# Performance work log

Measured on AMD Instinct MI355X. Metric: run time of the kernel, lower is better.

Reference implementation:

```python
import jax, jax.numpy as jnp
import numpy as np

H = 64
N_TYPES = 20
EDGE_DIM = 4
N_GRAPHS = 128
N_LAYERS = 3
N_NODES = 50000
N_EDGES = 800000
NQ = 4

# ---- quantum-circuit constants (4 qubits, statevector of 16) ----
def _cnot_mat(c, t, n=NQ):
    m = np.zeros((2**n, 2**n), np.complex64)
    for i in range(2**n):
        bits = [(i >> (n - 1 - k)) & 1 for k in range(n)]
        jb = list(bits)
        if bits[c]:
            jb[t] ^= 1
        j = sum(b << (n - 1 - k) for k, b in enumerate(jb))
        m[j, i] = 1.0
    return m

CNOTS = jnp.array(np.stack([_cnot_mat(q, (q + 1) % NQ) for q in range(NQ)]))
ZSIGN = jnp.array(np.array([[1.0 - 2.0 * ((i >> (NQ - 1 - q)) & 1) for i in range(2**NQ)] for q in range(NQ)], np.float32))
I2 = np.eye(2, dtype=np.complex64)

def _rx(t):
    c = jnp.cos(t / 2).astype(jnp.complex64)
    s = jnp.sin(t / 2).astype(jnp.complex64)
    return jnp.stack([jnp.stack([c, -1j * s]), jnp.stack([-1j * s, c])])

def _ry(t):
    c = jnp.cos(t / 2)
    s = jnp.sin(t / 2)
    return jnp.stack([jnp.stack([c, -s]), jnp.stack([s, c])]).astype(jnp.complex64)

def _full1q(g, q):
    ops = [jnp.asarray(I2)] * NQ
    ops[q] = g
    m = ops[0]
    for o in ops[1:]:
        m = jnp.kron(m, o)
    return m

def _circuit(x, w):
    # x: [4] input angles, w: [n_layers=2, 4] RY weights
    psi = jnp.zeros(2**NQ, jnp.complex64).at[0].set(1.0)
    for q in range(NQ):
        psi = _full1q(_rx(x[q]), q) @ psi
    for l in range(w.shape[0]):
        for q in range(NQ):
            psi = _full1q(_ry(w[l, q]), q) @ psi
        for q in range(NQ):
            psi = CNOTS[q] @ psi
    probs = jnp.abs(psi) ** 2
    return ZSIGN @ probs  # PauliZ expval per qubit, [4]

def _forward(node_types, edge_index, batch, pos, edge_attr, emb, ew1, eb1, ew2, eb2,
             cw1, cb1, cw2, cb2, nw1, nb1, nw2, nb2, prew, preb, qw, pw1, pb1, pw2, pb2):
    silu = jax.nn.silu
    n = pos.shape[0]
    src, dst = edge_index[0], edge_index[1]
    deg = jnp.maximum(jax.ops.segment_sum(jnp.ones((src.shape[0],), pos.dtype), dst, num_segments=n), 1.0)[:, None]
    h = emb[node_types]  # [N, H]
    for l in range(N_LAYERS):
        rel = pos[dst] - pos[src]                      # [E, 3]
        d2 = jnp.sum(rel * rel, axis=-1, keepdims=True)  # [E, 1]
        m_in = jnp.concatenate([h[dst], h[src], d2, edge_attr], axis=-1)  # [E, 2H+1+edge_dim]
        m = silu(m_in @ ew1[l] + eb1[l])
        m = silu(m @ ew2[l] + eb2[l])                  # [E, H] messages
        c = silu(m @ cw1[l] + cb1[l]) @ cw2[l] + cb2[l]  # [E, 1] coord scalar
        pos = pos + jax.ops.segment_sum(rel * c, dst, num_segments=n) / deg
        agg = jax.ops.segment_sum(m, dst, num_segments=n)  # [N, H]
        h = h + silu(jnp.concatenate([h, agg], axis=-1) @ nw1[l] + nb1[l]) @ nw2[l] + nb2[l]
    # global mean pool over graphs
    cnt = jnp.maximum(jax.ops.segment_sum(jnp.ones((n,), h.dtype), batch, num_segments=N_GRAPHS), 1.0)[:, None]
    g = jax.ops.segment_sum(h, batch, num_segments=N_GRAPHS) / cnt  # [G, H]
    q_in = g @ prew + preb                              # [G, 4]
    q_out = jax.vmap(lambda x: _circuit(x, qw))(q_in)   # [G, 4]
    return silu(q_out @ pw1 + pb1) @ pw2 + pb2          # [G, 1]

def setup_inputs() -> dict:
    key = jax.random.key(0)
    ks = jax.random.split(key, 20)
    def lin(k, i, o, layers=None):
        shape = (i, o) if layers is None else (layers, i, o)
        return (jax.random.normal(k, shape, jnp.float32) / np.sqrt(i))
    return {
        "node_types": jax.random.randint(ks[0], (N_NODES,), 0, N_TYPES),
        "pos": jax.random.normal(ks[1], (N_NODES, 3), jnp.float32),
        "edge_index": jax.random.randint(ks[2], (2, N_EDGES), 0, N_NODES),
        "edge_attr": jax.random.normal(ks[3], (N_EDGES, EDGE_DIM), jnp.float32),
        "batch": jnp.sort(jax.random.randint(ks[4], (N_NODES,), 0, N_GRAPHS)),
        "emb": jax.random.normal(ks[5], (N_TYPES, H), jnp.float32),
        "ew1": lin(ks[6], 2 * H + 1 + EDGE_DIM, H, N_LAYERS), "eb1": jnp.zeros((N_LAYERS, H), jnp.float32),
        "ew2": lin(ks[7], H, H, N_LAYERS), "eb2": jnp.zeros((N_LAYERS, H), jnp.float32),
        "cw1": lin(ks[8], H, H, N_LAYERS), "cb1": jnp.zeros((N_LAYERS, H), jnp.float32),
        "cw2": lin(ks[9], H, 1, N_LAYERS) * 0.1, "cb2": jnp.zeros((N_LAYERS, 1), jnp.float32),
        "nw1": lin(ks[10], 2 * H, H, N_LAYERS), "nb1": jnp.zeros((N_LAYERS, H), jnp.float32),
        "nw2": lin(ks[11], H, H, N_LAYERS), "nb2": jnp.zeros((N_LAYERS, H), jnp.float32),
        "prew": lin(ks[12], H, NQ), "preb": jnp.zeros((NQ,), jnp.float32),
        "qw": jax.random.uniform(ks[13], (2, NQ), jnp.float32, 0.0, 2.0 * np.pi),
        "pw1": lin(ks[14], NQ, H), "pb1": jnp.zeros((H,), jnp.float32),
        "pw2": lin(ks[15], H, 1), "pb2": jnp.zeros((1,), jnp.float32),
    }

def reference(node_types, pos, edge_index, edge_attr, batch, emb, ew1, eb1, ew2, eb2,
              cw1, cb1, cw2, cb2, nw1, nb1, nw2, nb2, prew, preb, qw, pw1, pb1, pw2, pb2):
    return _forward(node_types, edge_index, batch, pos, edge_attr, emb, ew1, eb1, ew2, eb2,
                    cw1, cb1, cw2, cb2, nw1, nb1, nw2, nb2, prew, preb, qw, pw1, pb1, pw2, pb2)
```

## Files before the change

### kernel.cpp

```cpp
#include <hip/hip_runtime.h>

#define NN 50000
#define NE 800000
#define NG 128
#define NL 3
#define NGRP (NE / 16)
#define SCANB ((NN + 1023) / 1024)

typedef __attribute__((ext_vector_type(8))) short short8;
typedef __attribute__((ext_vector_type(4))) float f32x4;
typedef __attribute__((ext_vector_type(4))) int i32x4;

union FragU { i32x4 i; short8 s; };

__device__ __forceinline__ float silu_f(float x) { return x / (1.f + __expf(-x)); }
__device__ __forceinline__ float rdl(float v, int l) {
  return __int_as_float(__builtin_amdgcn_readlane(__float_as_int(v), l));
}
__device__ __forceinline__ float wave_sum(float v) {
#pragma unroll
  for (int m = 1; m < 64; m <<= 1) v += __shfl_xor(v, m, 64);
  return v;
}

__device__ __forceinline__ unsigned f2u(float x) { return __float_as_uint(x); }
__device__ __forceinline__ float hi_part(float x) {
  return __uint_as_float(f2u(x) & 0xffff0000u);
}
__device__ __forceinline__ unsigned pk_hi(float e0, float e1) {
  return __builtin_amdgcn_perm(f2u(e1), f2u(e0), 0x07060302u);
}

__device__ __forceinline__ f32x4 mfma16(i32x4 a, i32x4 b, f32x4 c) {
  FragU ua, ub; ua.i = a; ub.i = b;
  return __builtin_amdgcn_mfma_f32_16x16x32_bf16(ua.s, ub.s, c, 0, 0, 0);
}

__device__ __forceinline__ void split8(const float* x, i32x4& fh, i32x4& fl) {
#pragma unroll
  for (int i = 0; i < 4; ++i) {
    const float a = x[2 * i], b = x[2 * i + 1];
    fh[i] = (int)pk_hi(a, b);
    fl[i] = (int)pk_hi(a - hi_part(a), b - hi_part(b));
  }
}

__device__ __forceinline__ void wfrag(const float* __restrict__ W, int nrows, int k0,
                                      int n, int lane, i32x4& fh, i32x4& fl) {
  const int kb = k0 + ((lane >> 4) << 3);
  float x[8];
#pragma unroll
  for (int j = 0; j < 8; ++j) {
    const int k = kb + j;
    x[j] = (k < nrows) ? W[k * 64 + n] : 0.f;
  }
  split8(x, fh, fl);
}

__global__ __launch_bounds__(256) void k_init_h(const int* __restrict__ nt,
                                                const float* __restrict__ emb,
                                                float* __restrict__ h,
                                                unsigned short* __restrict__ hpk) {
  int idx = blockIdx.x * 256 + threadIdx.x;
  if (idx < NN * 64) {
    const int node = idx >> 6, c = idx & 63;
    const float v = emb[nt[node] * 64 + c];
    h[idx] = v;
    const unsigned hb = f2u(v) & 0xffff0000u;
    const float lo = v - __uint_as_float(hb);
    hpk[node * 128 + c] = (unsigned short)(hb >> 16);
    hpk[node * 128 + 64 + c] = (unsigned short)(f2u(lo) >> 16);
  }
}

__global__ __launch_bounds__(256) void k_prep(const float* __restrict__ pos_in,
                                              float* __restrict__ pos,
                                              float* __restrict__ deg,
                                              float* __restrict__ g,
                                              float* __restrict__ gcnt,
                                              float* __restrict__ agg,
                                              float* __restrict__ posd) {
  int idx = blockIdx.x * 256 + threadIdx.x;
  if (idx < NN * 64) agg[idx] = 0.f;
  if (idx < NN * 3) { pos[idx] = pos_in[idx]; posd[idx] = 0.f; }
  if (idx < NN) deg[idx] = 0.f;
  if (idx < NG * 64) g[idx] = 0.f;
  if (idx < NG) gcnt[idx] = 0.f;
}

__global__ __launch_bounds__(256) void k_hist(const int* __restrict__ ei,
                                              float* __restrict__ deg) {
  int e = blockIdx.x * 256 + threadIdx.x;
  if (e < NE) atomicAdd(&deg[ei[NE + e]], 1.f);
}

__global__ __launch_bounds__(1024) void k_scanA(const float* __restrict__ deg,
                                                int* __restrict__ cursor,
                                                int* __restrict__ bsum) {
  __shared__ int wsum[16];
  const int tid = threadIdx.x, lane = tid & 63, w = tid >> 6;
  const int i = blockIdx.x * 1024 + tid;
  const int v = (i < NN) ? (int)deg[i] : 0;
  int x = v;
#pragma unroll
  for (int o = 1; o < 64; o <<= 1) {
    const int y = __shfl_up(x, o, 64);
    if (lane >= o) x += y;
  }
  if (lane == 63) wsum[w] = x;
  __syncthreads();
  if (tid == 0) {
    int acc = 0;
#pragma unroll
    for (int k = 0; k < 16; ++k) { const int t = wsum[k]; wsum[k] = acc; acc += t; }
    bsum[blockIdx.x] = acc;
  }
  __syncthreads();
  if (i < NN) cursor[i] = wsum[w] + (x - v);
}

__global__ __launch_bounds__(1024) void k_scanB(int* __restrict__ cursor,
                                                const int* __restrict__ bsum) {
  __shared__ int s_off;
  if (threadIdx.x == 0) {
    int a = 0;
    for (int k = 0; k < (int)blockIdx.x; ++k) a += bsum[k];
    s_off = a;
  }
  __syncthreads();
  const int i = blockIdx.x * 1024 + threadIdx.x;
  if (i < NN) cursor[i] += s_off;
}

__global__ __launch_bounds__(256) void k_scatter(const int* __restrict__ ei,
                                                 const float* __restrict__ eattr,
                                                 int* __restrict__ cursor,
                                                 int* __restrict__ ssrc,
                                                 int* __restrict__ sdst,
                                                 float4* __restrict__ seattr) {
  const int e = blockIdx.x * 256 + threadIdx.x;
  if (e < NE) {
    const int s = ei[e], d = ei[NE + e];
    const int p = atomicAdd(&cursor[d], 1);
    ssrc[p] = s;
    sdst[p] = d;
    seattr[p] = *(const float4*)(eattr + 4 * (size_t)e);
  }
}

__global__ __launch_bounds__(256) void k_cnt(const int* __restrict__ batch,
                                             float* __restrict__ deg,
                                             float* __restrict__ gcnt) {
  int i = blockIdx.x * 256 + threadIdx.x;
  if (i < NN) {
    deg[i] = fmaxf(deg[i], 1.f);
    atomicAdd(&gcnt[batch[i]], 1.f);
  }
}

__global__ __launch_bounds__(256) void k_pos(float* __restrict__ pos,
                                             float* __restrict__ posd,
                                             const float* __restrict__ deg) {
  int idx = blockIdx.x * 256 + threadIdx.x;
  if (idx < NN * 3) {
    pos[idx] += posd[idx] / deg[idx / 3];
    posd[idx] = 0.f;
  }
}

__global__ __launch_bounds__(256) void k_pool(const float* __restrict__ h,
                                              const int* __restrict__ batch,
                                              float* __restrict__ g) {
  const int lane = threadIdx.x & 63;
  const int wid = (blockIdx.x * 256 + threadIdx.x) >> 6;
  const int nw = (gridDim.x * 256) >> 6;
  for (int n0 = wid * 16; n0 < NN; n0 += nw * 16) {
    float acc = 0.f;
    int curb = batch[n0];
#pragma unroll
    for (int i = 0; i < 16; ++i) {
      const int b = batch[n0 + i];
      const float v = h[(size_t)(n0 + i) * 64 + lane];
      if (b != curb) {
        atomicAdd(&g[curb * 64 + lane], acc);
        acc = 0.f;
        curb = b;
      }
      acc += v;
    }
    atomicAdd(&g[curb * 64 + lane], acc);
  }
}

#define STORE_PAIR(base, row, toff, v)                                          \
  {                                                                             \
    const float vp_ = __shfl_xor((v), 1, 64);                                   \
    if (!(m & 1)) {                                                             \
      const int off_ = (row) * 128 + ((((toff) + m * 2)) ^ (((row) & 7) << 4)); \
      *(unsigned*)((base) + off_) = pk_hi((v), vp_);                            \
      *(unsigned*)((base) + 2048 + off_) =                                      \
          pk_hi((v)-hi_part(v), vp_ - hi_part(vp_));                            \
    }                                                                           \
  }

__global__ __launch_bounds__(768, 3) void k_edge(
    const unsigned short* __restrict__ hpk, const float* __restrict__ pos,
    const int* __restrict__ ssrc, const int* __restrict__ sdst,
    const float4* __restrict__ seattr,
    const float* __restrict__ W1, const float* __restrict__ B1,
    const float* __restrict__ W2, const float* __restrict__ B2,
    const float* __restrict__ C1, const float* __restrict__ CB1,
    const float* __restrict__ C2, const float* __restrict__ CB2,
    float* __restrict__ agg, float* __restrict__ posd) {
  __shared__ i32x4 smem[7680];

  const int tid = threadIdx.x;
  const int lane = tid & 63;
  const int w = tid >> 6;
  const int m = lane & 15;
  const int quad = lane >> 4;

  for (int j = w; j < 36; j += 12) {
    int s, t, nrows, hb, lb;
    const float* W;
    if (j < 20)      { s = j >> 2; t = j & 3; W = W1; nrows = 133; hb = 0; lb = 1280; }
    else if (j < 28) { const int q = j - 20; s = q >> 2; t = q & 3; W = W2; nrows = 64; hb = 2560; lb = 3072; }
    else             { const int q = j - 28; s = q >> 2; t = q & 3; W = C1; nrows = 64; hb = 3584; lb = 4096; }
    i32x4 fh, fl;
    wfrag(W, nrows, 32 * s, t * 16 + m, lane, fh, fl);
    smem[hb + (s * 4 + t) * 64 + lane] = fh;
    smem[lb + (s * 4 + t) * 64 + lane] = fl;
  }
  __syncthreads();

  float eb1t[4], eb2t[4], cb1t[4], cw2t[4];
#pragma unroll
  for (int t = 0; t < 4; ++t) {
    eb1t[t] = B1[t * 16 + m];
    eb2t[t] = B2[t * 16 + m];
    cb1t[t] = CB1[t * 16 + m];
    cw2t[t] = C2[t * 16 + m];
  }
  const float cb2v = CB2[0];

  char* pl = (char*)(smem + 4608) + w * 4096;
  const char* hB = (const char*)hpk;

  const int gw = blockIdx.x * 12 + w;
  const int nwv = gridDim.x * 12;
  const int ipw = (NGRP + nwv - 1) / nwv;
  const int gbeg = min(gw * ipw, NGRP);
  const int gend = min(gbeg + ipw, NGRP);

  int es = 0, ed = 0;
  if (gbeg < gend) {
    es = ssrc[gbeg * 16 + m];
    ed = sdst[gbeg * 16 + m];
  }

  for (int g = gbeg; g < gend; ++g) {
    const int e0 = g * 16;
    const int ces = es, ced = ed;
    if (g + 1 < gend) {
      es = ssrc[(g + 1) * 16 + m];
      ed = sdst[(g + 1) * 16 + m];
    }

    i32x4 fh[4], fl[4];
#pragma unroll
    for (int s = 0; s < 4; ++s) {
      const unsigned node = (unsigned)(s < 2 ? ced : ces);
      const unsigned off = node * 256u + (unsigned)((s & 1) * 64 + quad * 16);
      fh[s] = *(const i32x4*)(hB + off);
      fl[s] = *(const i32x4*)(hB + off + 128);
    }

    float rx = 0.f, ry = 0.f, rz = 0.f, d2v = 0.f;
    float ea0 = 0.f, ea1 = 0.f, ea2 = 0.f, ea3 = 0.f;
    if (lane < 16) {
      rx = pos[ced * 3 + 0] - pos[ces * 3 + 0];
      ry = pos[ced * 3 + 1] - pos[ces * 3 + 1];
      rz = pos[ced * 3 + 2] - pos[ces * 3 + 2];
      d2v = rx * rx + ry * ry + rz * rz;
      const float4 ea = seattr[e0 + lane];
      ea0 = ea.x; ea1 = ea.y; ea2 = ea.z; ea3 = ea.w;
    }

    i32x4 th, tl;
    {
      float x0 = __shfl(d2v, m), x1 = __shfl(ea0, m), x2 = __shfl(ea1, m),
            x3 = __shfl(ea2, m), x4 = __shfl(ea3, m);
      if (quad) { x0 = x1 = x2 = x3 = x4 = 0.f; }
      float xt[8] = {x0, x1, x2, x3, x4, 0.f, 0.f, 0.f};
      split8(xt, th, tl);
    }

#pragma unroll
    for (int t = 0; t < 4; ++t) {
      f32x4 P = {eb1t[t], eb1t[t], eb1t[t], eb1t[t]}, Q = {0.f, 0.f, 0.f, 0.f};
#pragma unroll
      for (int s = 0; s < 4; ++s) {
        const i32x4 wh = smem[(s * 4 + t) * 64 + lane];
        const i32x4 wl = smem[1280 + (s * 4 + t) * 64 + lane];
        P = mfma16(fh[s], wh, P);
        Q = mfma16(fh[s], wl, Q);
        Q = mfma16(fl[s], wh, Q);
      }
      {
        const i32x4 wh = smem[(16 + t) * 64 + lane];
        const i32x4 wl = smem[1280 + (16 + t) * 64 + lane];
        P = mfma16(th, wh, P);
        Q = mfma16(th, wl, Q);
        Q = mfma16(tl, wh, Q);
      }
#pragma unroll
      for (int r = 0; r < 4; ++r) {
        const int row = quad * 4 + r;
        const float v = silu_f(P[r] + Q[r]);
        STORE_PAIR(pl, row, t * 32, v);
      }
    }

    i32x4 ah[2], al[2];
#pragma unroll
    for (int s = 0; s < 2; ++s) {
      const int off = m * 128 + ((s * 64 + quad * 16) ^ ((m & 7) << 4));
      ah[s] = *(const i32x4*)(pl + off);
      al[s] = *(const i32x4*)(pl + 2048 + off);
    }
    float mv[4][4];
#pragma unroll
    for (int t = 0; t < 4; ++t) {
      f32x4 P = {eb2t[t], eb2t[t], eb2t[t], eb2t[t]}, Q = {0.f, 0.f, 0.f, 0.f};
#pragma unroll
      for (int s = 0; s < 2; ++s) {
        const i32x4 wh = smem[2560 + (s * 4 + t) * 64 + lane];
        const i32x4 wl = smem[3072 + (s * 4 + t) * 64 + lane];
        P = mfma16(ah[s], wh, P);
        Q = mfma16(ah[s], wl, Q);
        Q = mfma16(al[s], wh, Q);
      }
#pragma unroll
      for (int r = 0; r < 4; ++r) {
        const int row = quad * 4 + r;
        mv[t][r] = silu_f(P[r] + Q[r]);
        STORE_PAIR(pl, row, t * 32, mv[t][r]);
      }
    }

    {
      const bool headp = (m == 0) || (ced != __shfl(ced, lane - 1, 64));
      unsigned rem = (unsigned)(__ballot(headp) & 0xFFFFull);
      while (rem) {
        const int hrow = __ffs((int)rem) - 1;
        rem &= rem - 1;
        const int nrow = rem ? (__ffs((int)rem) - 1) : 16;
        const int dstn = __shfl(ced, hrow, 64);
#pragma unroll
        for (int t = 0; t < 4; ++t) {
          float s = 0.f;
#pragma unroll
          for (int r = 0; r < 4; ++r) {
            const int row = quad * 4 + r;
            s += (row >= hrow && row < nrow) ? mv[t][r] : 0.f;
          }
          s += __shfl_xor(s, 16, 64);
          s += __shfl_xor(s, 32, 64);
          if (quad == 0) atomicAdd(&agg[(size_t)dstn * 64 + t * 16 + m], s);
        }
      }
    }

    i32x4 mh[2], ml[2];
#pragma unroll
    for (int s = 0; s < 2; ++s) {
      const int off = m * 128 + ((s * 64 + quad * 16) ^ ((m & 7) << 4));
      mh[s] = *(const i32x4*)(pl + off);
      ml[s] = *(const i32x4*)(pl + 2048 + off);
    }
    float tr[4] = {0.f, 0.f, 0.f, 0.f};
#pragma unroll
    for (int t = 0; t < 4; ++t) {
      f32x4 P = {cb1t[t], cb1t[t], cb1t[t], cb1t[t]}, Q = {0.f, 0.f, 0.f, 0.f};
#pragma unroll
      for (int s = 0; s < 2; ++s) {
        const i32x4 wh = smem[3584 + (s * 4 + t) * 64 + lane];
        const i32x4 wl = smem[4096 + (s * 4 + t) * 64 + lane];
        P = mfma16(mh[s], wh, P);
        Q = mfma16(mh[s], wl, Q);
        Q = mfma16(ml[s], wh, Q);
      }
#pragma unroll
      for (int r = 0; r < 4; ++r) tr[r] += silu_f(P[r] + Q[r]) * cw2t[t];
    }
#pragma unroll
    for (int mask = 1; mask < 16; mask <<= 1)
#pragma unroll
      for (int r = 0; r < 4; ++r) tr[r] += __shfl_xor(tr[r], mask, 64);

    {
      const int rr = m >> 2, cc = m & 3;
      const int e = quad * 4 + rr;
      const float tv = ((rr & 2) ? ((rr & 1) ? tr[3] : tr[2])
                                 : ((rr & 1) ? tr[1] : tr[0])) + cb2v;
      const int d_ = __shfl(ced, e, 64);
      const float ax = __shfl(rx, e, 64), ay = __shfl(ry, e, 64),
                  az = __shfl(rz, e, 64);
      if (cc < 3) {
        const float rel = cc == 0 ? ax : (cc == 1 ? ay : az);
        atomicAdd(&posd[d_ * 3 + cc], rel * tv);
      }
    }
  }
}

__global__ __launch_bounds__(256) void k_node(
    float* __restrict__ h, unsigned short* __restrict__ hpk,
    float* __restrict__ agg,
    const float* __restrict__ W1, const float* __restrict__ B1,
    const float* __restrict__ W2, const float* __restrict__ B2) {
  __shared__ float sW1[128 * 64];
  __shared__ float sW2[64 * 64];
  for (int i = threadIdx.x; i < 128 * 64; i += 256) sW1[i] = W1[i];
  for (int i = threadIdx.x; i < 64 * 64; i += 256) sW2[i] = W2[i];
  __syncthreads();
  const int lane = threadIdx.x & 63;
  const float nb1 = B1[lane], nb2 = B2[lane];
  const int wid = (blockIdx.x * 256 + threadIdx.x) >> 6;
  const int nw = (gridDim.x * 256) >> 6;
  for (int n0 = wid * 8; n0 < NN; n0 += nw * 8) {
    float hj[8], aj[8], a1[8];
#pragma unroll
    for (int i = 0; i < 8; ++i) {
      hj[i] = h[(size_t)(n0 + i) * 64 + lane];
      aj[i] = agg[(size_t)(n0 + i) * 64 + lane];
      a1[i] = nb1;
    }
#pragma unroll
    for (int i = 0; i < 8; ++i) agg[(size_t)(n0 + i) * 64 + lane] = 0.f;
#pragma unroll
    for (int k = 0; k < 64; ++k) {
      const float wv = sW1[k * 64 + lane];
#pragma unroll
      for (int i = 0; i < 8; ++i) a1[i] += rdl(hj[i], k) * wv;
    }
#pragma unroll
    for (int k = 0; k < 64; ++k) {
      const float wv = sW1[(64 + k) * 64 + lane];
#pragma unroll
      for (int i = 0; i < 8; ++i) a1[i] += rdl(aj[i], k) * wv;
    }
    float u[8], a2[8];
#pragma unroll
    for (int i = 0; i < 8; ++i) { u[i] = silu_f(a1[i]); a2[i] = nb2; }
#pragma unroll
    for (int k = 0; k < 64; ++k) {
      const float wv = sW2[k * 64 + lane];
#pragma unroll
      for (int i = 0; i < 8; ++i) a2[i] += rdl(u[i], k) * wv;
    }
#pragma unroll
    for (int i = 0; i < 8; ++i) {
      const float hn = hj[i] + a2[i];
      h[(size_t)(n0 + i) * 64 + lane] = hn;
      const unsigned hb = f2u(hn) & 0xffff0000u;
      const float lo = hn - __uint_as_float(hb);
      hpk[(size_t)(n0 + i) * 128 + lane] = (unsigned short)(hb >> 16);
      hpk[(size_t)(n0 + i) * 128 + 64 + lane] = (unsigned short)(f2u(lo) >> 16);
    }
  }
}

__global__ __launch_bounds__(256) void k_final(
    const float* __restrict__ g, const float* __restrict__ gcnt,
    const float* __restrict__ prew, const float* __restrict__ preb,
    const float* __restrict__ qw, const float* __restrict__ pw1,
    const float* __restrict__ pb1, const float* __restrict__ pw2,
    const float* __restrict__ pb2, float* __restrict__ out) {
  const int lane = threadIdx.x & 63;
  const int gid = (blockIdx.x * 256 + threadIdx.x) >> 6;
  if (gid >= NG) return;
  const float cnt = fmaxf(gcnt[gid], 1.f);
  const float gv = g[gid * 64 + lane] / cnt;
  float qin[4];
#pragma unroll
  for (int q = 0; q < 4; ++q)
    qin[q] = wave_sum(gv * prew[lane * 4 + q]) + preb[q];
  float sr[16], si[16];
#pragma unroll
  for (int i = 0; i < 16; ++i) { sr[i] = 0.f; si[i] = 0.f; }
  sr[0] = 1.f;
#pragma unroll
  for (int q = 0; q < 4; ++q) {
    const int mask = 8 >> q;
    float s, c;
    __sincosf(qin[q] * 0.5f, &s, &c);
#pragma unroll
    for (int i = 0; i < 16; ++i)
      if (!(i & mask)) {
        const int j = i | mask;
        const float ar = sr[i], ai = si[i], br = sr[j], bi = si[j];
        sr[i] = c * ar + s * bi; si[i] = c * ai - s * br;
        sr[j] = c * br + s * ai; si[j] = c * bi - s * ar;
      }
  }
#pragma unroll
  for (int l = 0; l < 2; ++l) {
#pragma unroll
    for (int q = 0; q < 4; ++q) {
      const int mask = 8 >> q;
      float s, c;
      __sincosf(qw[l * 4 + q] * 0.5f, &s, &c);
#pragma unroll
      for (int i = 0; i < 16; ++i)
        if (!(i & mask)) {
          const int j = i | mask;
          const float ar = sr[i], ai = si[i], br = sr[j], bi = si[j];
          sr[i] = c * ar - s * br; si[i] = c * ai - s * bi;
          sr[j] = s * ar + c * br; si[j] = s * ai + c * bi;
        }
    }
#pragma unroll
    for (int q = 0; q < 4; ++q) {
      const int mc = 8 >> q;
      const int mt = 8 >> ((q + 1) & 3);
#pragma unroll
      for (int i = 0; i < 16; ++i)
        if ((i & mc) && !(i & mt)) {
          const int j = i | mt;
          float t = sr[i]; sr[i] = sr[j]; sr[j] = t;
          t = si[i]; si[i] = si[j]; si[j] = t;
        }
    }
  }
  float qo[4] = {0.f, 0.f, 0.f, 0.f};
#pragma unroll
  for (int i = 0; i < 16; ++i) {
    const float p = sr[i] * sr[i] + si[i] * si[i];
#pragma unroll
    for (int q = 0; q < 4; ++q) qo[q] += ((i >> (3 - q)) & 1) ? -p : p;
  }
  float t = pb1[lane];
#pragma unroll
  for (int q = 0; q < 4; ++q) t += qo[q] * pw1[q * 64 + lane];
  const float r = wave_sum(silu_f(t) * pw2[lane]);
  if (lane == 0) out[gid] = r + pb2[0];
}

extern "C" void kernel_launch(void* const* d_in, const int* in_sizes, int n_in,
                              void* d_out, int out_size, void* d_ws, size_t ws_size,
                              hipStream_t stream) {
  (void)in_sizes; (void)n_in; (void)out_size; (void)ws_size;
  const int*   nt    = (const int*)d_in[0];
  const float* pos0  = (const float*)d_in[1];
  const int*   ei    = (const int*)d_in[2];
  const float* eattr = (const float*)d_in[3];
  const int*   batch = (const int*)d_in[4];
  const float* emb   = (const float*)d_in[5];
  const float* ew1   = (const float*)d_in[6];
  const float* eb1   = (const float*)d_in[7];
  const float* ew2   = (const float*)d_in[8];
  const float* eb2   = (const float*)d_in[9];
  const float* cw1   = (const float*)d_in[10];
  const float* cb1   = (const float*)d_in[11];
  const float* cw2   = (const float*)d_in[12];
  const float* cb2   = (const float*)d_in[13];
  const float* nw1   = (const float*)d_in[14];
  const float* nb1   = (const float*)d_in[15];
  const float* nw2   = (const float*)d_in[16];
  const float* nb2   = (const float*)d_in[17];
  const float* prew  = (const float*)d_in[18];
  const float* preb  = (const float*)d_in[19];
  const float* qw    = (const float*)d_in[20];
  const float* pw1   = (const float*)d_in[21];
  const float* pb1   = (const float*)d_in[22];
  const float* pw2   = (const float*)d_in[23];
  const float* pb2   = (const float*)d_in[24];
  float* out = (float*)d_out;

  float* ws   = (float*)d_ws;
  float* h    = ws;
  float* pos  = h + NN * 64;
  float* posd = pos + NN * 3;
  float* agg  = posd + NN * 3;
  float* deg  = agg + NN * 64;
  float* g    = deg + NN;
  float* gcnt = g + NG * 64;
  unsigned short* hpk = (unsigned short*)(gcnt + NG);
  float4* seattr = (float4*)(hpk + NN * 128);
  int* ssrc   = (int*)(seattr + NE);
  int* sdst   = ssrc + NE;
  int* cursor = sdst + NE;
  int* bsum   = cursor + NN;

  k_init_h<<<(NN * 64 + 255) / 256, 256, 0, stream>>>(nt, emb, h, hpk);
  k_prep<<<(NN * 64 + 255) / 256, 256, 0, stream>>>(pos0, pos, deg, g, gcnt,
                                                    agg, posd);
  k_hist<<<(NE + 255) / 256, 256, 0, stream>>>(ei, deg);
  k_scanA<<<SCANB, 1024, 0, stream>>>(deg, cursor, bsum);
  k_scanB<<<SCANB, 1024, 0, stream>>>(cursor, bsum);
  k_scatter<<<(NE + 255) / 256, 256, 0, stream>>>(ei, eattr, cursor, ssrc, sdst,
                                                  seattr);
  k_cnt<<<(NN + 255) / 256, 256, 0, stream>>>(batch, deg, gcnt);
  for (int l = 0; l < NL; ++l) {
    k_edge<<<256, 768, 0, stream>>>(hpk, pos, ssrc, sdst, seattr,
        ew1 + l * 133 * 64, eb1 + l * 64, ew2 + l * 64 * 64, eb2 + l * 64,
        cw1 + l * 64 * 64, cb1 + l * 64, cw2 + l * 64, cb2 + l, agg, posd);
    k_pos<<<(NN * 3 + 255) / 256, 256, 0, stream>>>(pos, posd, deg);
    k_node<<<512, 256, 0, stream>>>(h, hpk, agg, nw1 + l * 128 * 64, nb1 + l * 64,
                                    nw2 + l * 64 * 64, nb2 + l * 64);
  }
  k_pool<<<800, 256, 0, stream>>>(h, batch, g);
  k_final<<<(NG * 64 + 255) / 256, 256, 0, stream>>>(g, gcnt, prew, preb, qw,
                                                     pw1, pb1, pw2, pb2, out);
}
```

Before: 1.075 ms.

## Process two 16-edge groups per wave iteration in edge kernel; fuse pooling and init

The edge kernel now handles 32 edges per loop iteration, running the first-layer MFMAs for two groups together. The goal is more independent loads and MFMA work in flight to hide gather and matrix latency, at the cost of higher register pressure. Graph pooling is folded into the last node-update kernel and the init/prep kernels are merged, which removes two launches and one full pass over h.

```diff
diff --git a/kernel.cpp b/kernel.cpp
--- a/kernel.cpp
+++ b/kernel.cpp
@@ -4,7 +4,7 @@
 #define NE 800000
 #define NG 128
 #define NL 3
-#define NGRP (NE / 16)
+#define NPAIR (NE / 32)
 #define SCANB ((NN + 1023) / 1024)
 
 typedef __attribute__((ext_vector_type(8))) short short8;
@@ -57,12 +57,20 @@
   split8(x, fh, fl);
 }
 
-__global__ __launch_bounds__(256) void k_init_h(const int* __restrict__ nt,
-                                                const float* __restrict__ emb,
-                                                float* __restrict__ h,
-                                                unsigned short* __restrict__ hpk) {
+__global__ __launch_bounds__(256) void k_prep(const int* __restrict__ nt,
+                                              const float* __restrict__ emb,
+                                              const float* __restrict__ pos_in,
+                                              float* __restrict__ pos,
+                                              float* __restrict__ deg,
+                                              float* __restrict__ g,
+                                              float* __restrict__ gcnt,
+                                              float* __restrict__ agg,
+                                              float* __restrict__ posd,
+                                              float* __restrict__ h,
+                                              unsigned short* __restrict__ hpk) {
   int idx = blockIdx.x * 256 + threadIdx.x;
   if (idx < NN * 64) {
+    agg[idx] = 0.f;
     const int node = idx >> 6, c = idx & 63;
     const float v = emb[nt[node] * 64 + c];
     h[idx] = v;
@@ -71,17 +79,6 @@
     hpk[node * 128 + c] = (unsigned short)(hb >> 16);
     hpk[node * 128 + 64 + c] = (unsigned short)(f2u(lo) >> 16);
   }
-}
-
-__global__ __launch_bounds__(256) void k_prep(const float* __restrict__ pos_in,
-                                              float* __restrict__ pos,
-                                              float* __restrict__ deg,
-                                              float* __restrict__ g,
-                                              float* __restrict__ gcnt,
-                                              float* __restrict__ agg,
-                                              float* __restrict__ posd) {
-  int idx = blockIdx.x * 256 + threadIdx.x;
-  if (idx < NN * 64) agg[idx] = 0.f;
   if (idx < NN * 3) { pos[idx] = pos_in[idx]; posd[idx] = 0.f; }
   if (idx < NN) deg[idx] = 0.f;
   if (idx < NG * 64) g[idx] = 0.f;
@@ -168,30 +165,6 @@
   }
 }
 
-__global__ __launch_bounds__(256) void k_pool(const float* __restrict__ h,
-                                              const int* __restrict__ batch,
-                                              float* __restrict__ g) {
-  const int lane = threadIdx.x & 63;
-  const int wid = (blockIdx.x * 256 + threadIdx.x) >> 6;
-  const int nw = (gridDim.x * 256) >> 6;
-  for (int n0 = wid * 16; n0 < NN; n0 += nw * 16) {
-    float acc = 0.f;
-    int curb = batch[n0];
-#pragma unroll
-    for (int i = 0; i < 16; ++i) {
-      const int b = batch[n0 + i];
-      const float v = h[(size_t)(n0 + i) * 64 + lane];
-      if (b != curb) {
-        atomicAdd(&g[curb * 64 + lane], acc);
-        acc = 0.f;
-        curb = b;
-      }
-      acc += v;
-    }
-    atomicAdd(&g[curb * 64 + lane], acc);
-  }
-}
-
 #define STORE_PAIR(base, row, toff, v)                                          \
   {                                                                             \
     const float vp_ = __shfl_xor((v), 1, 64);                                   \
@@ -248,167 +221,289 @@
 
   const int gw = blockIdx.x * 12 + w;
   const int nwv = gridDim.x * 12;
-  const int ipw = (NGRP + nwv - 1) / nwv;
-  const int gbeg = min(gw * ipw, NGRP);
-  const int gend = min(gbeg + ipw, NGRP);
-
-  int es = 0, ed = 0;
+  const int ipw = (NPAIR + nwv - 1) / nwv;
+  const int gbeg = min(gw * ipw, NPAIR);
+  const int gend = min(gbeg + ipw, NPAIR);
+
+  int esA = 0, edA = 0, esB = 0, edB = 0;
   if (gbeg < gend) {
-    es = ssrc[gbeg * 16 + m];
-    ed = sdst[gbeg * 16 + m];
+    const int b = gbeg * 32 + m;
+    esA = ssrc[b]; edA = sdst[b]; esB = ssrc[b + 16]; edB = sdst[b + 16];
   }
 
   for (int g = gbeg; g < gend; ++g) {
-    const int e0 = g * 16;
-    const int ces = es, ced = ed;
+    const int e0 = g * 32;
+    const int cesA = esA, cedA = edA, cesB = esB, cedB = edB;
     if (g + 1 < gend) {
-      es = ssrc[(g + 1) * 16 + m];
-      ed = sdst[(g + 1) * 16 + m];
-    }
-
-    i32x4 fh[4], fl[4];
+      const int b = (g + 1) * 32 + m;
+      esA = ssrc[b]; edA = sdst[b]; esB = ssrc[b + 16]; edB = sdst[b + 16];
+    }
+
+    i32x4 fha[4], fla[4], fhb[4], flb[4];
 #pragma unroll
     for (int s = 0; s < 4; ++s) {
-      const unsigned node = (unsigned)(s < 2 ? ced : ces);
+      const unsigned node = (unsigned)(s < 2 ? cedA : cesA);
       const unsigned off = node * 256u + (unsigned)((s & 1) * 64 + quad * 16);
-      fh[s] = *(const i32x4*)(hB + off);
-      fl[s] = *(const i32x4*)(hB + off + 128);
+      fha[s] = *(const i32x4*)(hB + off);
+      fla[s] = *(const i32x4*)(hB + off + 128);
+    }
+#pragma unroll
+    for (int s = 0; s < 4; ++s) {
+      const unsigned node = (unsigned)(s < 2 ? cedB : cesB);
+      const unsigned off = node * 256u + (unsigned)((s & 1) * 64 + quad * 16);
+      fhb[s] = *(const i32x4*)(hB + off);
+      flb[s] = *(const i32x4*)(hB + off + 128);
     }
 
     float rx = 0.f, ry = 0.f, rz = 0.f, d2v = 0.f;
     float ea0 = 0.f, ea1 = 0.f, ea2 = 0.f, ea3 = 0.f;
-    if (lane < 16) {
-      rx = pos[ced * 3 + 0] - pos[ces * 3 + 0];
-      ry = pos[ced * 3 + 1] - pos[ces * 3 + 1];
-      rz = pos[ced * 3 + 2] - pos[ces * 3 + 2];
+    if (lane < 32) {
+      const int s_ = (lane < 16) ? cesA : cesB;
+      const int d_ = (lane < 16) ? cedA : cedB;
+      rx = pos[d_ * 3 + 0] - pos[s_ * 3 + 0];
+      ry = pos[d_ * 3 + 1] - pos[s_ * 3 + 1];
+      rz = pos[d_ * 3 + 2] - pos[s_ * 3 + 2];
       d2v = rx * rx + ry * ry + rz * rz;
       const float4 ea = seattr[e0 + lane];
       ea0 = ea.x; ea1 = ea.y; ea2 = ea.z; ea3 = ea.w;
     }
 
-    i32x4 th, tl;
+    i32x4 thA, tlA, thB, tlB;
     {
       float x0 = __shfl(d2v, m), x1 = __shfl(ea0, m), x2 = __shfl(ea1, m),
             x3 = __shfl(ea2, m), x4 = __shfl(ea3, m);
       if (quad) { x0 = x1 = x2 = x3 = x4 = 0.f; }
       float xt[8] = {x0, x1, x2, x3, x4, 0.f, 0.f, 0.f};
-      split8(xt, th, tl);
-    }
-
+      split8(xt, thA, tlA);
+    }
+    {
+      float x0 = __shfl(d2v, 16 + m), x1 = __shfl(ea0, 16 + m),
+            x2 = __shfl(ea1, 16 + m), x3 = __shfl(ea2, 16 + m),
+            x4 = __shfl(ea3, 16 + m);
+      if (quad) { x0 = x1 = x2 = x3 = x4 = 0.f; }
+      float xt[8] = {x0, x1, x2, x3, x4, 0.f, 0.f, 0.f};
+      split8(xt, thB, tlB);
+    }
+
+    float m1B[4][4];
 #pragma unroll
     for (int t = 0; t < 4; ++t) {
-      f32x4 P = {eb1t[t], eb1t[t], eb1t[t], eb1t[t]}, Q = {0.f, 0.f, 0.f, 0.f};
+      f32x4 PA = {eb1t[t], eb1t[t], eb1t[t], eb1t[t]}, QA = {0.f, 0.f, 0.f, 0.f};
+      f32x4 PB = {eb1t[t], eb1t[t], eb1t[t], eb1t[t]}, QB = {0.f, 0.f, 0.f, 0.f};
 #pragma unroll
       for (int s = 0; s < 4; ++s) {
         const i32x4 wh = smem[(s * 4 + t) * 64 + lane];
         const i32x4 wl = smem[1280 + (s * 4 + t) * 64 + lane];
-        P = mfma16(fh[s], wh, P);
-        Q = mfma16(fh[s], wl, Q);
-        Q = mfma16(fl[s], wh, Q);
+        PA = mfma16(fha[s], wh, PA);
+        QA = mfma16(fha[s], wl, QA);
+        QA = mfma16(fla[s], wh, QA);
+        PB = mfma16(fhb[s], wh, PB);
+        QB = mfma16(fhb[s], wl, QB);
+        QB = mfma16(flb[s], wh, QB);
       }
       {
         const i32x4 wh = smem[(16 + t) * 64 + lane];
         const i32x4 wl = smem[1280 + (16 + t) * 64 + lane];
-        P = mfma16(th, wh, P);
-        Q = mfma16(th, wl, Q);
-        Q = mfma16(tl, wh, Q);
+        PA = mfma16(thA, wh, PA);
+        QA = mfma16(thA, wl, QA);
+        QA = mfma16(tlA, wh, QA);
+        PB = mfma16(thB, wh, PB);
+        QB = mfma16(thB, wl, QB);
+        QB = mfma16(tlB, wh, QB);
       }
 #pragma unroll
       for (int r = 0; r < 4; ++r) {
         const int row = quad * 4 + r;
-        const float v = silu_f(P[r] + Q[r]);
-        STORE_PAIR(pl, row, t * 32, v);
-      }
-    }
-
-    i32x4 ah[2], al[2];
-#pragma unroll
-    for (int s = 0; s < 2; ++s) {
-      const int off = m * 128 + ((s * 64 + quad * 16) ^ ((m & 7) << 4));
-      ah[s] = *(const i32x4*)(pl + off);
-      al[s] = *(const i32x4*)(pl + 2048 + off);
-    }
-    float mv[4][4];
-#pragma unroll
-    for (int t = 0; t < 4; ++t) {
-      f32x4 P = {eb2t[t], eb2t[t], eb2t[t], eb2t[t]}, Q = {0.f, 0.f, 0.f, 0.f};
+        const float vA = silu_f(PA[r] + QA[r]);
+        STORE_PAIR(pl, row, t * 32, vA);
+        m1B[t][r] = silu_f(PB[r] + QB[r]);
+      }
+    }
+
+    {
+      i32x4 ah[2], al[2];
 #pragma unroll
       for (int s = 0; s < 2; ++s) {
-        const i32x4 wh = smem[2560 + (s * 4 + t) * 64 + lane];
-        const i32x4 wl = smem[3072 + (s * 4 + t) * 64 + lane];
-        P = mfma16(ah[s], wh, P);
-        Q = mfma16(ah[s], wl, Q);
-        Q = mfma16(al[s], wh, Q);
-      }
-#pragma unroll
-      for (int r = 0; r < 4; ++r) {
-        const int row = quad * 4 + r;
-        mv[t][r] = silu_f(P[r] + Q[r]);
-        STORE_PAIR(pl, row, t * 32, mv[t][r]);
+        const int off = m * 128 + ((s * 64 + quad * 16) ^ ((m & 7) << 4));
+        ah[s] = *(const i32x4*)(pl + off);
+        al[s] = *(const i32x4*)(pl + 2048 + off);
+      }
+      float mv[4][4];
+#pragma unroll
+      for (int t = 0; t < 4; ++t) {
+        f32x4 P = {eb2t[t], eb2t[t], eb2t[t], eb2t[t]}, Q = {0.f, 0.f, 0.f, 0.f};
+#pragma unroll
+        for (int s = 0; s < 2; ++s) {
+          const i32x4 wh = smem[2560 + (s * 4 + t) * 64 + lane];
+          const i32x4 wl = smem[3072 + (s * 4 + t) * 64 + lane];
+          P = mfma16(ah[s], wh, P);
+          Q = mfma16(ah[s], wl, Q);
+          Q = mfma16(al[s], wh, Q);
+        }
+#pragma unroll
+        for (int r = 0; r < 4; ++r) {
+          const int row = quad * 4 + r;
+          mv[t][r] = silu_f(P[r] + Q[r]);
+          STORE_PAIR(pl, row, t * 32, mv[t][r]);
+        }
+      }
+      {
+        const bool headp = (m == 0) || (cedA != __shfl(cedA, lane - 1, 64));
+        unsigned rem = (unsigned)(__ballot(headp) & 0xFFFFull);
+        while (rem) {
+          const int hrow = __ffs((int)rem) - 1;
+          rem &= rem - 1;
+          const int nrow = rem ? (__ffs((int)rem) - 1) : 16;
+          const int dstn = __shfl(cedA, hrow, 64);
+#pragma unroll
+          for (int t = 0; t < 4; ++t) {
+            float s = 0.f;
+#pragma unroll
+            for (int r = 0; r < 4; ++r) {
+              const int row = quad * 4 + r;
+              s += (row >= hrow && row < nrow) ? mv[t][r] : 0.f;
+            }
+            s += __shfl_xor(s, 16, 64);
+            s += __shfl_xor(s, 32, 64);
+            if (quad == 0) atomicAdd(&agg[(size_t)dstn * 64 + t * 16 + m], s);
+          }
+        }
+      }
+      i32x4 mh[2], ml[2];
+#pragma unroll
+      for (int s = 0; s < 2; ++s) {
+        const int off = m * 128 + ((s * 64 + quad * 16) ^ ((m & 7) << 4));
+        mh[s] = *(const i32x4*)(pl + off);
+        ml[s] = *(const i32x4*)(pl + 2048 + off);
+      }
+      float tr[4] = {0.f, 0.f, 0.f, 0.f};
+#pragma unroll
+      for (int t = 0; t < 4; ++t) {
+        f32x4 P = {cb1t[t], cb1t[t], cb1t[t], cb1t[t]}, Q = {0.f, 0.f, 0.f, 0.f};
+#pragma unroll
+        for (int s = 0; s < 2; ++s) {
+          const i32x4 wh = smem[3584 + (s * 4 + t) * 64 + lane];
+          const i32x4 wl = smem[4096 + (s * 4 + t) * 64 + lane];
+          P = mfma16(mh[s], wh, P);
+          Q = mfma16(mh[s], wl, Q);
+          Q = mfma16(ml[s], wh, Q);
+        }
+#pragma unroll
+        for (int r = 0; r < 4; ++r) tr[r] += silu_f(P[r] + Q[r]) * cw2t[t];
+      }
+#pragma unroll
+      for (int mask = 1; mask < 16; mask <<= 1)
+#pragma unroll
+        for (int r = 0; r < 4; ++r) tr[r] += __shfl_xor(tr[r], mask, 64);
+      {
+        const int rr = m >> 2, cc = m & 3;
+        const int e = quad * 4 + rr;
+        const float tv = ((rr & 2) ? ((rr & 1) ? tr[3] : tr[2])
+                                   : ((rr & 1) ? tr[1] : tr[0])) + cb2v;
+        const int d_ = __shfl(cedA, e, 64);
+        const float ax = __shfl(rx, e, 64), ay = __shfl(ry, e, 64),
+                    az = __shfl(rz, e, 64);
+        if (cc < 3) {
+          const float rel = cc == 0 ? ax : (cc == 1 ? ay : az);
+          atomicAdd(&posd[d_ * 3 + cc], rel * tv);
+        }
       }
     }
 
     {
-      const bool headp = (m == 0) || (ced != __shfl(ced, lane - 1, 64));
-      unsigned rem = (unsigned)(__ballot(headp) & 0xFFFFull);
-      while (rem) {
-        const int hrow = __ffs((int)rem) - 1;
-        rem &= rem - 1;
-        const int nrow = rem ? (__ffs((int)rem) - 1) : 16;
-        const int dstn = __shfl(ced, hrow, 64);
-#pragma unroll
-        for (int t = 0; t < 4; ++t) {
-          float s = 0.f;
-#pragma unroll
-          for (int r = 0; r < 4; ++r) {
-            const int row = quad * 4 + r;
-            s += (row >= hrow && row < nrow) ? mv[t][r] : 0.f;
+#pragma unroll
+      for (int t = 0; t < 4; ++t)
+#pragma unroll
+        for (int r = 0; r < 4; ++r) {
+          const int row = quad * 4 + r;
+          STORE_PAIR(pl, row, t * 32, m1B[t][r]);
+        }
+      i32x4 ah[2], al[2];
+#pragma unroll
+      for (int s = 0; s < 2; ++s) {
+        const int off = m * 128 + ((s * 64 + quad * 16) ^ ((m & 7) << 4));
+        ah[s] = *(const i32x4*)(pl + off);
+        al[s] = *(const i32x4*)(pl + 2048 + off);
+      }
+      float mv[4][4];
+#pragma unroll
+      for (int t = 0; t < 4; ++t) {
+        f32x4 P = {eb2t[t], eb2t[t], eb2t[t], eb2t[t]}, Q = {0.f, 0.f, 0.f, 0.f};
+#pragma unroll
+        for (int s = 0; s < 2; ++s) {
+          const i32x4 wh = smem[2560 + (s * 4 + t) * 64 + lane];
+          const i32x4 wl = smem[3072 + (s * 4 + t) * 64 + lane];
+          P = mfma16(ah[s], wh, P);
+          Q = mfma16(ah[s], wl, Q);
+          Q = mfma16(al[s], wh, Q);
+        }
+#pragma unroll
+        for (int r = 0; r < 4; ++r) {
+          const int row = quad * 4 + r;
+          mv[t][r] = silu_f(P[r] + Q[r]);
+          STORE_PAIR(pl, row, t * 32, mv[t][r]);
+        }
+      }
+      {
+        const bool headp = (m == 0) || (cedB != __shfl(cedB, lane - 1, 64));
+        unsigned rem = (unsigned)(__ballot(headp) & 0xFFFFull);
+        while (rem) {
+          const int hrow = __ffs((int)rem) - 1;
+          rem &= rem - 1;
+          const int nrow = rem ? (__ffs((int)rem) - 1) : 16;
+          const int dstn = __shfl(cedB, hrow, 64);
+#pragma unroll
+          for (int t = 0; t < 4; ++t) {
+            float s = 0.f;
+#pragma unroll
+            for (int r = 0; r < 4; ++r) {
+              const int row = quad * 4 + r;
+              s += (row >= hrow && row < nrow) ? mv[t][r] : 0.f;
+            }
+            s += __shfl_xor(s, 16, 64);
+            s += __shfl_xor(s, 32, 64);
+            if (quad == 0) atomicAdd(&agg[(size_t)dstn * 64 + t * 16 + m], s);
           }
-          s += __shfl_xor(s, 16, 64);
-          s += __shfl_xor(s, 32, 64);
-          if (quad == 0) atomicAdd(&agg[(size_t)dstn * 64 + t * 16 + m], s);
-        }
-      }
-    }
-
-    i32x4 mh[2], ml[2];
-#pragma unroll
-    for (int s = 0; s < 2; ++s) {
-      const int off = m * 128 + ((s * 64 + quad * 16) ^ ((m & 7) << 4));
-      mh[s] = *(const i32x4*)(pl + off);
-      ml[s] = *(const i32x4*)(pl + 2048 + off);
-    }
-    float tr[4] = {0.f, 0.f, 0.f, 0.f};
-#pragma unroll
-    for (int t = 0; t < 4; ++t) {
-      f32x4 P = {cb1t[t], cb1t[t], cb1t[t], cb1t[t]}, Q = {0.f, 0.f, 0.f, 0.f};
+        }
+      }
+      i32x4 mh[2], ml[2];
 #pragma unroll
       for (int s = 0; s < 2; ++s) {
-        const i32x4 wh = smem[3584 + (s * 4 + t) * 64 + lane];
-        const i32x4 wl = smem[4096 + (s * 4 + t) * 64 + lane];
-        P = mfma16(mh[s], wh, P);
-        Q = mfma16(mh[s], wl, Q);
-        Q = mfma16(ml[s], wh, Q);
-      }
-#pragma unroll
-      for (int r = 0; r < 4; ++r) tr[r] += silu_f(P[r] + Q[r]) * cw2t[t];
-    }
-#pragma unroll
-    for (int mask = 1; mask < 16; mask <<= 1)
-#pragma unroll
-      for (int r = 0; r < 4; ++r) tr[r] += __shfl_xor(tr[r], mask, 64);
-
-    {
-      const int rr = m >> 2, cc = m & 3;
-      const int e = quad * 4 + rr;
-      const float tv = ((rr & 2) ? ((rr & 1) ? tr[3] : tr[2])
-                                 : ((rr & 1) ? tr[1] : tr[0])) + cb2v;
-      const int d_ = __shfl(ced, e, 64);
-      const float ax = __shfl(rx, e, 64), ay = __shfl(ry, e, 64),
-                  az = __shfl(rz, e, 64);
-      if (cc < 3) {
-        const float rel = cc == 0 ? ax : (cc == 1 ? ay : az);
-        atomicAdd(&posd[d_ * 3 + cc], rel * tv);
+        const int off = m * 128 + ((s * 64 + quad * 16) ^ ((m & 7) << 4));
+        mh[s] = *(const i32x4*)(pl + off);
+        ml[s] = *(const i32x4*)(pl + 2048 + off);
+      }
+      float tr[4] = {0.f, 0.f, 0.f, 0.f};
+#pragma unroll
+      for (int t = 0; t < 4; ++t) {
+        f32x4 P = {cb1t[t], cb1t[t], cb1t[t], cb1t[t]}, Q = {0.f, 0.f, 0.f, 0.f};
+#pragma unroll
+        for (int s = 0; s < 2; ++s) {
+          const i32x4 wh = smem[3584 + (s * 4 + t) * 64 + lane];
+          const i32x4 wl = smem[4096 + (s * 4 + t) * 64 + lane];
+          P = mfma16(mh[s], wh, P);
+          Q = mfma16(mh[s], wl, Q);
+          Q = mfma16(ml[s], wh, Q);
+        }
+#pragma unroll
+        for (int r = 0; r < 4; ++r) tr[r] += silu_f(P[r] + Q[r]) * cw2t[t];
+      }
+#pragma unroll
+      for (int mask = 1; mask < 16; mask <<= 1)
+#pragma unroll
+        for (int r = 0; r < 4; ++r) tr[r] += __shfl_xor(tr[r], mask, 64);
+      {
+        const int rr = m >> 2, cc = m & 3;
+        const int e = quad * 4 + rr;
+        const float tv = ((rr & 2) ? ((rr & 1) ? tr[3] : tr[2])
+                                   : ((rr & 1) ? tr[1] : tr[0])) + cb2v;
+        const int d_ = __shfl(cedB, e, 64);
+        const float ax = __shfl(rx, 16 + e, 64), ay = __shfl(ry, 16 + e, 64),
+                    az = __shfl(rz, 16 + e, 64);
+        if (cc < 3) {
+          const float rel = cc == 0 ? ax : (cc == 1 ? ay : az);
+          atomicAdd(&posd[d_ * 3 + cc], rel * tv);
+        }
       }
     }
   }
@@ -418,7 +513,8 @@
     float* __restrict__ h, unsigned short* __restrict__ hpk,
     float* __restrict__ agg,
     const float* __restrict__ W1, const float* __restrict__ B1,
-    const float* __restrict__ W2, const float* __restrict__ B2) {
+    const float* __restrict__ W2, const float* __restrict__ B2,
+    const int* __restrict__ batch, float* __restrict__ gpool) {
   __shared__ float sW1[128 * 64];
   __shared__ float sW2[64 * 64];
   for (int i = threadIdx.x; i < 128 * 64; i += 256) sW1[i] = W1[i];
@@ -459,14 +555,30 @@
 #pragma unroll
       for (int i = 0; i < 8; ++i) a2[i] += rdl(u[i], k) * wv;
     }
+    float hn[8];
 #pragma unroll
     for (int i = 0; i < 8; ++i) {
-      const float hn = hj[i] + a2[i];
-      h[(size_t)(n0 + i) * 64 + lane] = hn;
-      const unsigned hb = f2u(hn) & 0xffff0000u;
-      const float lo = hn - __uint_as_float(hb);
+      hn[i] = hj[i] + a2[i];
+      h[(size_t)(n0 + i) * 64 + lane] = hn[i];
+      const unsigned hb = f2u(hn[i]) & 0xffff0000u;
+      const float lo = hn[i] - __uint_as_float(hb);
       hpk[(size_t)(n0 + i) * 128 + lane] = (unsigned short)(hb >> 16);
       hpk[(size_t)(n0 + i) * 128 + 64 + lane] = (unsigned short)(f2u(lo) >> 16);
+    }
+    if (gpool) {
+      float acc = 0.f;
+      int curb = batch[n0];
+#pragma unroll
+      for (int i = 0; i < 8; ++i) {
+        const int b = batch[n0 + i];
+        if (b != curb) {
+          atomicAdd(&gpool[curb * 64 + lane], acc);
+          acc = 0.f;
+          curb = b;
+        }
+        acc += hn[i];
+      }
+      atomicAdd(&gpool[curb * 64 + lane], acc);
     }
   }
 }
@@ -593,9 +705,8 @@
   int* cursor = sdst + NE;
   int* bsum   = cursor + NN;
 
-  k_init_h<<<(NN * 64 + 255) / 256, 256, 0, stream>>>(nt, emb, h, hpk);
-  k_prep<<<(NN * 64 + 255) / 256, 256, 0, stream>>>(pos0, pos, deg, g, gcnt,
-                                                    agg, posd);
+  k_prep<<<(NN * 64 + 255) / 256, 256, 0, stream>>>(nt, emb, pos0, pos, deg, g,
+                                                    gcnt, agg, posd, h, hpk);
   k_hist<<<(NE + 255) / 256, 256, 0, stream>>>(ei, deg);
   k_scanA<<<SCANB, 1024, 0, stream>>>(deg, cursor, bsum);
   k_scanB<<<SCANB, 1024, 0, stream>>>(cursor, bsum);
@@ -608,9 +719,9 @@
         cw1 + l * 64 * 64, cb1 + l * 64, cw2 + l * 64, cb2 + l, agg, posd);
     k_pos<<<(NN * 3 + 255) / 256, 256, 0, stream>>>(pos, posd, deg);
     k_node<<<512, 256, 0, stream>>>(h, hpk, agg, nw1 + l * 128 * 64, nb1 + l * 64,
-                                    nw2 + l * 64 * 64, nb2 + l * 64);
-  }
-  k_pool<<<800, 256, 0, stream>>>(h, batch, g);
+                                    nw2 + l * 64 * 64, nb2 + l * 64, batch,
+                                    (l == NL - 1) ? g : nullptr);
+  }
   k_final<<<(NG * 64 + 255) / 256, 256, 0, stream>>>(g, gcnt, prew, preb, qw,
                                                      pw1, pb1, pw2, pb2, out);
 }
```

After: 1.679 ms. +56.2%, slower.
